# Performance work log

Hardware: AMD Instinct MI355X
Metric: run time of the kernel (lower is better)

## Reference

```python
import jax, jax.numpy as jnp
import numpy as np

BS, T, G, C = 64, 128, 36, 256
H = 256          # gaze LSTM hidden
P = 256          # spatial projected size
PT = 256         # temporal projected size
Q = 16           # queue size
NC = 10          # num classes
NEG = -1e9


def setup_inputs() -> dict:
    key = jax.random.key(0)
    ks = jax.random.split(key, 40)
    s = 0.02
    D = C + H
    inp = {
        'cnn_feat_seq': jax.random.normal(ks[0], (BS, T, G, C), jnp.float32),
        'gaze_seq': jax.random.normal(ks[1], (BS, T, 3), jnp.float32),
        # init-hidden / init-cell MLPs (Linear(3,H), Tanh, Linear(H,H), Tanh)
        'init_h_w1': jax.random.normal(ks[2], (H, 3)) * s, 'init_h_b1': jnp.zeros((H,)),
        'init_h_w2': jax.random.normal(ks[3], (H, H)) * s, 'init_h_b2': jnp.zeros((H,)),
        'init_c_w1': jax.random.normal(ks[4], (H, 3)) * s, 'init_c_b1': jnp.zeros((H,)),
        'init_c_w2': jax.random.normal(ks[5], (H, H)) * s, 'init_c_b2': jnp.zeros((H,)),
        # LSTM (input 3, hidden H), torch gate order i,f,g,o
        'lstm_wih': jax.random.normal(ks[6], (4 * H, 3)) * s, 'lstm_whh': jax.random.normal(ks[7], (4 * H, H)) * s,
        'lstm_bih': jnp.zeros((4 * H,)), 'lstm_bhh': jnp.zeros((4 * H,)),
        # spatial attention
        'sa_wl': jax.random.normal(ks[8], (P, H)) * s, 'sa_bl': jnp.zeros((P,)),
        'sa_wc': jax.random.normal(ks[9], (P, C)) * s, 'sa_bc': jnp.zeros((P,)),
        'sa_wz': jax.random.normal(ks[10], (P,)) * s,
        # temporal attention
        'ta_wl': jax.random.normal(ks[11], (PT, H)) * s, 'ta_bl': jnp.zeros((PT,)),
        'ta_wv': jax.random.normal(ks[12], (PT, C)) * s, 'ta_bv': jnp.zeros((PT,)),
        'ta_wz': jax.random.normal(ks[13], (PT,)) * s,
        # MLP classifier: Linear(D,D) -> Linear(D,D) -> Linear(D,NC), no nonlinearity
        'mlp_w1': jax.random.normal(ks[14], (D, D)) * s, 'mlp_b1': jnp.zeros((D,)),
        'mlp_w2': jax.random.normal(ks[15], (D, D)) * s, 'mlp_b2': jnp.zeros((D,)),
        'mlp_w3': jax.random.normal(ks[16], (NC, D)) * s, 'mlp_b3': jnp.zeros((NC,)),
    }
    return inp


def _forward(cnn_feat_seq, gaze_seq,
             init_h_w1, init_h_b1, init_h_w2, init_h_b2,
             init_c_w1, init_c_b1, init_c_w2, init_c_b2,
             lstm_wih, lstm_whh, lstm_bih, lstm_bhh,
             sa_wl, sa_bl, sa_wc, sa_bc, sa_wz,
             ta_wl, ta_bl, ta_wv, ta_bv, ta_wz,
             mlp_w1, mlp_b1, mlp_w2, mlp_b2, mlp_w3, mlp_b3):
    bs, num_frame = gaze_seq.shape[0], gaze_seq.shape[1]
    mean_gaze = jnp.mean(gaze_seq, axis=1)  # (bs, 3)
    # init MLP ends with Tanh, and forward applies F.tanh again
    h0 = jnp.tanh(jnp.tanh(jnp.tanh(mean_gaze @ init_h_w1.T + init_h_b1) @ init_h_w2.T + init_h_b2))
    c0 = jnp.tanh(jnp.tanh(jnp.tanh(mean_gaze @ init_c_w1.T + init_c_b1) @ init_c_w2.T + init_c_b2))
    buf_s0 = jnp.zeros((Q, bs, C), cnn_feat_seq.dtype)
    buf_h0 = jnp.zeros((Q, bs, H), cnn_feat_seq.dtype)
    qidx = jnp.arange(Q)

    def step(carry, xs):
        h, c, buf_s, buf_h, i = carry
        feat, gaze = xs  # (bs,G,C), (bs,3)
        # --- spatial additive attention over grids ---
        Hp = h @ sa_wl.T + sa_bl                                  # (bs,P)
        Vp = jnp.einsum('bgc,pc->bgp', feat, sa_wc) + sa_bc       # (bs,G,P)
        zs = jnp.tanh(Hp[:, None, :] + Vp) @ sa_wz                # (bs,G)
        sw = jax.nn.softmax(zs, axis=1)
        spat = jnp.einsum('bgc,bg->bc', feat, sw)                 # (bs,C)
        # --- rolling queues (newest last) ---
        buf_s = jnp.concatenate([buf_s[1:], spat[None]], axis=0)
        buf_h = jnp.concatenate([buf_h[1:], h[None]], axis=0)
        count = jnp.minimum(i + 1, Q)
        mask = qidx >= (Q - count)                                # (Q,) valid slots
        # --- temporal additive attention over queue ---
        Hq = jnp.einsum('qbh,ph->qbp', buf_h, ta_wl) + ta_bl
        Vq = jnp.einsum('qbc,pc->qbp', buf_s, ta_wv) + ta_bv
        zt = jnp.tanh(Hq + Vq) @ ta_wz                            # (Q,bs)
        zt = jnp.where(mask[:, None], zt, NEG)
        tw = jax.nn.softmax(zt, axis=0)
        temp = jnp.einsum('qbc,qb->bc', buf_s, tw)                # (bs,C)
        # --- one LSTM step on gaze ---
        gates = gaze @ lstm_wih.T + lstm_bih + h @ lstm_whh.T + lstm_bhh
        gi, gf, gg, go = jnp.split(gates, 4, axis=-1)
        c = jax.nn.sigmoid(gf) * c + jax.nn.sigmoid(gi) * jnp.tanh(gg)
        h = jax.nn.sigmoid(go) * jnp.tanh(c)
        # --- classifier on concat(temporal_feat, lstm_hidden) ---
        fc = jnp.concatenate([temp, h], axis=1)                   # (bs, C+H)
        pred = ((fc @ mlp_w1.T + mlp_b1) @ mlp_w2.T + mlp_b2) @ mlp_w3.T + mlp_b3
        return (h, c, buf_s, buf_h, i + 1), pred

    feats_t = jnp.swapaxes(cnn_feat_seq, 0, 1)  # (T,bs,G,C)
    gaze_t = jnp.swapaxes(gaze_seq, 0, 1)       # (T,bs,3)
    _, preds = jax.lax.scan(step, (h0, c0, buf_s0, buf_h0, jnp.int32(0)), (feats_t, gaze_t))
    # torch cats (1,bs,NC) pieces along dim=1 -> (1, T*bs, NC)
    return preds.reshape(1, num_frame * bs, NC)


def reference(cnn_feat_seq, gaze_seq,
              init_h_w1, init_h_b1, init_h_w2, init_h_b2,
              init_c_w1, init_c_b1, init_c_w2, init_c_b2,
              lstm_wih, lstm_whh, lstm_bih, lstm_bhh,
              sa_wl, sa_bl, sa_wc, sa_bc, sa_wz,
              ta_wl, ta_bl, ta_wv, ta_bv, ta_wz,
              mlp_w1, mlp_b1, mlp_w2, mlp_b2, mlp_w3, mlp_b3):
    return _forward(cnn_feat_seq, gaze_seq,
                    init_h_w1, init_h_b1, init_h_w2, init_h_b2,
                    init_c_w1, init_c_b1, init_c_w2, init_c_b2,
                    lstm_wih, lstm_whh, lstm_bih, lstm_bhh,
                    sa_wl, sa_bl, sa_wc, sa_bc, sa_wz,
                    ta_wl, ta_bl, ta_wv, ta_bv, ta_wz,
                    mlp_w1, mlp_b1, mlp_w2, mlp_b2, mlp_w3, mlp_b3)
```

## Files before the change

### kernel.cpp

```cpp
#include <hip/hip_runtime.h>
#include <cstdint>
#include <cstddef>

#define BSZ 64
#define TT  128
#define GG  36
#define CC  256
#define HH  256
#define QQ  16
#define NCLS 10
#define NROW 8192
#define SP_ROWS 16

using short8  = __attribute__((ext_vector_type(8))) short;
using f32x4   = __attribute__((ext_vector_type(4))) float;
using half2_t = __attribute__((ext_vector_type(2))) _Float16;
typedef unsigned int u32;
typedef unsigned short u16;

#define OFF_WI    0u
#define OFF_WF    131072u
#define OFF_WG    262144u
#define OFF_WO    393216u
#define OFF_SAWL  524288u
#define OFF_TAWL  655360u
#define OFF_TAWV  786432u
#define OFF_SAWC  917504u
#define OFF_W32   1048576u
#define OFF_WC    1069056u
#define OFF_BC    1089536u
#define OFF_H0F16 1089792u
#define OFF_C0    1122560u
#define OFF_HSEQ  1188096u
#define OFF_HSEQB 9642240u
#define OFF_HPSA  13869312u
#define OFF_HQ    22257920u
#define OFF_SPAT  30646528u
#define OFF_SPATB 39035136u
#define OFF_ZSC   43229440u
#define WS_NEEDED 43262208u
#define OFF_FEATB 43262208u
#define WS_NEED_BIG 194257152u

__device__ __forceinline__ float rcp_fast(float x){
#if __has_builtin(__builtin_amdgcn_rcpf)
  return __builtin_amdgcn_rcpf(x);
#else
  return 1.f/x;
#endif
}
__device__ __forceinline__ float fast_sig(float x){ return rcp_fast(1.f+__expf(-x)); }
__device__ __forceinline__ float fast_tanh(float x){ float e=__expf(2.f*x); return 1.f-2.f*rcp_fast(e+1.f); }
__device__ __forceinline__ u16 f2bf(float f){
  u32 u = __builtin_bit_cast(u32, f);
  u += 0x7fffu + ((u>>16)&1u);
  return (u16)(u>>16);
}
__device__ __forceinline__ float bf2f(u16 b){
  u32 u = ((u32)b)<<16; return __builtin_bit_cast(float, u);
}
__device__ __forceinline__ u32 cvtpk_bf16(float a, float b){
  u32 p;
  asm("v_cvt_pk_bf16_f32 %0, %1, %2" : "=v"(p) : "v"(a), "v"(b));
  return p;
}
__device__ __forceinline__ u32 packf16(float a, float b){
  half2_t h; h.x = (_Float16)a; h.y = (_Float16)b;
  return __builtin_bit_cast(u32, h);
}
__device__ __forceinline__ float dot2(u32 w, u32 h, float acc){
#if __has_builtin(__builtin_amdgcn_fdot2)
  return __builtin_amdgcn_fdot2(__builtin_bit_cast(half2_t, w),
                                __builtin_bit_cast(half2_t, h), acc, false);
#else
  half2_t a = __builtin_bit_cast(half2_t, w), b = __builtin_bit_cast(half2_t, h);
  return acc + (float)a.x*(float)b.x + (float)a.y*(float)b.y;
#endif
}
__device__ __forceinline__ f32x4 mfma16(short8 a, short8 b, f32x4 c){
  return __builtin_amdgcn_mfma_f32_16x16x32_bf16(a, b, c, 0, 0, 0);
}

__global__ void __launch_bounds__(256) k_prep1(const float* __restrict__ whh,
    const float* __restrict__ sawl, const float* __restrict__ tawl,
    const float* __restrict__ tawv, const float* __restrict__ sawc,
    const float* __restrict__ w3, const float* __restrict__ w2, char* ws){
  int blk = blockIdx.x, tid = threadIdx.x;
  if (blk < 512){
    u32* wq = (u32*)ws;
    for (int rr = 0; rr < 2; ++rr){
      int row = blk*2 + rr;
      float v  = whh[row*256 + tid];
      float vn = __shfl_down(v, 1);
      if ((tid & 1) == 0){
        int typ = row >> 8;
        int j   = row & 255;
        wq[typ*32768 + (tid>>1)*256 + j] = packf16(v, vn);
      }
    }
  } else if (blk < 544){
    int rel = blk - 512;
    int mat = rel >> 3;
    const float* src; u16* dst;
    if (mat==0){ src=sawl; dst=(u16*)(ws+OFF_SAWL); }
    else if (mat==1){ src=tawl; dst=(u16*)(ws+OFF_TAWL); }
    else if (mat==2){ src=tawv; dst=(u16*)(ws+OFF_TAWV); }
    else { src=sawc; dst=(u16*)(ws+OFF_SAWC); }
    int base = (rel & 7)*8192 + tid;
    if (mat < 3){
      for (int i = 0; i < 32; ++i){ int e = base + i*256; dst[e] = f2bf(src[e]); }
    } else {
      for (int i = 0; i < 32; ++i){
        int e = base + i*256;
        int col = e >> 8, kk = e & 255;
        dst[col*256 + (kk ^ ((col&7)<<3))] = f2bf(src[e]);
      }
    }
  } else {
    int idx = (blk-544)*256 + tid;
    int o = idx >> 9, k2 = idx & 511;
    float acc = 0.f;
    for (int m = 0; m < 512; ++m) acc = fmaf(w3[o*512+m], w2[m*512+k2], acc);
    ((float*)(ws+OFF_W32))[idx] = acc;
  }
}

__global__ void __launch_bounds__(256) k_prep2(const float* __restrict__ w1,
    const float* __restrict__ b1, const float* __restrict__ w3,
    const float* __restrict__ b2, const float* __restrict__ b3,
    const float* __restrict__ gaze,
    const float* __restrict__ ihw1, const float* __restrict__ ihb1,
    const float* __restrict__ ihw2, const float* __restrict__ ihb2,
    const float* __restrict__ icw1, const float* __restrict__ icb1,
    const float* __restrict__ icw2, const float* __restrict__ icb2,
    char* ws){
  int blk = blockIdx.x, tid = threadIdx.x;
  const float* W32 = (const float*)(ws+OFF_W32);
  if (blk < 20){
    int idx = blk*256 + tid; int o = idx>>9, k = idx&511;
    float acc = 0.f;
    for (int m = 0; m < 512; ++m) acc = fmaf(W32[o*512+m], w1[m*512+k], acc);
    ((float*)(ws+OFF_WC))[idx] = acc;
  } else if (blk == 20){
    if (tid < 10){
      float acc = b3[tid];
      for (int m = 0; m < 512; ++m) acc = fmaf(W32[tid*512+m], b1[m], acc);
      for (int m = 0; m < 512; ++m) acc = fmaf(w3[tid*512+m], b2[m], acc);
      ((float*)(ws+OFF_BC))[tid] = acc;
    }
  } else {
    int b = blk - 21;
    __shared__ float red0[128], red1[128], red2[128];
    __shared__ float mg[3];
    __shared__ float x1[256];
    if (tid < 128){
      const float* gp = gaze + b*384 + tid*3;
      red0[tid] = gp[0]; red1[tid] = gp[1]; red2[tid] = gp[2];
    }
    __syncthreads();
    for (int s = 64; s >= 1; s >>= 1){
      if (tid < s){ red0[tid]+=red0[tid+s]; red1[tid]+=red1[tid+s]; red2[tid]+=red2[tid+s]; }
      __syncthreads();
    }
    if (tid == 0){ mg[0]=red0[0]*(1.f/128.f); mg[1]=red1[0]*(1.f/128.f); mg[2]=red2[0]*(1.f/128.f); }
    __syncthreads();
    for (int which = 0; which < 2; ++which){
      const float* aw1 = which? icw1 : ihw1; const float* ab1 = which? icb1 : ihb1;
      const float* aw2 = which? icw2 : ihw2; const float* ab2 = which? icb2 : ihb2;
      float v = fast_tanh(fmaf(aw1[tid*3+2],mg[2], fmaf(aw1[tid*3+1],mg[1], fmaf(aw1[tid*3],mg[0], ab1[tid]))));
      x1[tid] = v;
      __syncthreads();
      float acc = ab2[tid];
      for (int k = 0; k < 256; ++k) acc = fmaf(aw2[tid*256+k], x1[k], acc);
      float h0 = fast_tanh(fast_tanh(acc));
      if (which == 0){
        float* hseq = (float*)(ws+OFF_HSEQ);
        hseq[(size_t)(0*64 + b)*256 + tid] = h0;
        float hn = __shfl_down(h0, 1);
        if ((tid&1)==0){
          ((u32*)(ws+OFF_HSEQB))[((size_t)(0*64+b)*256 + tid)>>1] = ((u32)f2bf(hn)<<16) | f2bf(h0);
          ((u32*)(ws+OFF_H0F16))[b*128 + (tid>>1)] = packf16(h0, hn);
        }
      } else {
        ((float*)(ws+OFF_C0))[b*256 + tid] = h0;
      }
      __syncthreads();
    }
  }
}

__global__ void __launch_bounds__(512, 2) k_lstm_vp(const float* __restrict__ gaze,
    const float* __restrict__ wih, const float* __restrict__ bih,
    const float* __restrict__ bhh, const float* __restrict__ feat, char* ws){
  __shared__ u32 lds_w[16*2048];
  __shared__ __align__(16) u32 hbuf[2][128];
  __shared__ float p_lds[256];
  __shared__ float g_lds[384];
  int tid = threadIdx.x;

  if (blockIdx.x >= 64){
    int cb = blockIdx.x - 64;
    u32* fbg = (u32*)(ws + OFF_FEATB);
    for (int r = cb; r < NROW; r += 192){
      int t = r >> 6, b = r & 63;
      const float4* fb = (const float4*)(feat + ((size_t)(b*128 + t))*9216);
      u32* dst = fbg + (size_t)r*4608;
#pragma unroll
      for (int ii = 0; ii < 4; ++ii){
        int e = tid + ii*512;
        float4 v = fb[e];
        int g = e >> 6, c4 = e & 63;
        uint2 pp;
        pp.x = cvtpk_bf16(v.x, v.y);
        pp.y = cvtpk_bf16(v.z, v.w);
        *reinterpret_cast<uint2*>(dst + g*128 + ((c4*2) ^ ((g&7)<<2))) = pp;
      }
      if (tid < 256){
        int e = 2048 + tid;
        float4 v = fb[e];
        int g = e >> 6, c4 = e & 63;
        uint2 pp;
        pp.x = cvtpk_bf16(v.x, v.y);
        pp.y = cvtpk_bf16(v.z, v.w);
        *reinterpret_cast<uint2*>(dst + g*128 + ((c4*2) ^ ((g&7)<<2))) = pp;
      }
    }
    return;
  }

  int b = blockIdx.x;
  int half = tid >> 8;
  int j = tid & 255;

  const u32* wq = (const u32*)ws;
  const u32* wA = wq + (half ? 1 : 0) * 32768;
  const u32* wB = wq + (half ? 3 : 2) * 32768;
  u32 w0[128], w1r[64];
#pragma unroll
  for (int c = 0; c < 128; ++c) w0[c] = wA[c*256 + j];
#pragma unroll
  for (int c = 0; c < 64; ++c)  w1r[c] = wB[c*256 + j];
#pragma unroll
  for (int cq = 0; cq < 16; ++cq)
#pragma unroll
    for (int q = 0; q < 4; ++q)
      lds_w[cq*2048 + tid*4 + q] = wB[(64 + cq*4 + q)*256 + j];

  if (tid < 384) g_lds[tid] = gaze[b*384 + tid];
  if (tid < 128) hbuf[0][tid] = ((const u32*)(ws+OFF_H0F16))[b*128 + tid];
  float creg = half ? ((const float*)(ws+OFF_C0))[b*256 + j] : 0.f;

  int rA = half ? 256 + j : j;
  int rB = half ? 768 + j : 512 + j;
  float baseA = bih[rA] + bhh[rA];
  float baseB = bih[rB] + bhh[rB];
  float uA0 = wih[rA*3], uA1 = wih[rA*3+1], uA2 = wih[rA*3+2];
  float uB0 = wih[rB*3], uB1 = wih[rB*3+1], uB2 = wih[rB*3+2];

  float* hseq = (float*)(ws+OFF_HSEQ);
  u32* hseqb = (u32*)(ws+OFF_HSEQB);
  float hv_prev = 0.f; u32 hpk_prev = 0;
  __syncthreads();

  for (int t = 0; t < 128; ++t){
    int cur = t & 1, nxt = cur ^ 1;
    if (half == 1 && t > 0){
      hseq[((size_t)t*64 + b)*256 + j] = hv_prev;
      if ((j & 1) == 0)
        hseqb[(((size_t)t*64 + b)*256 + j)>>1] = hpk_prev;
    }
    float g0 = g_lds[t*3], g1 = g_lds[t*3+1], g2 = g_lds[t*3+2];
    float aA0 = fmaf(uA2,g2, fmaf(uA1,g1, fmaf(uA0,g0, baseA))), aA1 = 0.f;
    float aB0 = fmaf(uB2,g2, fmaf(uB1,g1, fmaf(uB0,g0, baseB))), aB1 = 0.f;
#pragma unroll
    for (int c4 = 0; c4 < 32; ++c4){
      uint4 h4 = *reinterpret_cast<const uint4*>(&hbuf[cur][c4*4]);
      u32 wb0, wb1, wb2, wb3;
      if (c4 < 16){
        wb0 = w1r[c4*4]; wb1 = w1r[c4*4+1]; wb2 = w1r[c4*4+2]; wb3 = w1r[c4*4+3];
      } else {
        uint4 wv = *reinterpret_cast<const uint4*>(&lds_w[(c4-16)*2048 + tid*4]);
        wb0 = wv.x; wb1 = wv.y; wb2 = wv.z; wb3 = wv.w;
      }
      aA0 = dot2(w0[c4*4+0], h4.x, aA0); aB0 = dot2(wb0, h4.x, aB0);
      aA1 = dot2(w0[c4*4+1], h4.y, aA1); aB1 = dot2(wb1, h4.y, aB1);
      aA0 = dot2(w0[c4*4+2], h4.z, aA0); aB0 = dot2(wb2, h4.z, aB0);
      aA1 = dot2(w0[c4*4+3], h4.w, aA1); aB1 = dot2(wb3, h4.w, aB1);
    }
    float aA = aA0 + aA1, aB = aB0 + aB1;
    if (half == 0){
      p_lds[j] = fast_sig(aA) * fast_tanh(aB);
    }
    __syncthreads();
    if (half == 1){
      float p = p_lds[j];
      creg = fmaf(fast_sig(aA), creg, p);
      float hv = fast_sig(aB) * fast_tanh(creg);
      float hn = __shfl_down(hv, 1);
      if ((j & 1) == 0) hbuf[nxt][j>>1] = packf16(hv, hn);
      hv_prev = hv;
      hpk_prev = ((u32)f2bf(hn)<<16) | f2bf(hv);
    }
    __syncthreads();
  }
  if (half == 1){
    hseq[((size_t)128*64 + b)*256 + j] = hv_prev;
    if ((j & 1) == 0)
      hseqb[(((size_t)128*64 + b)*256 + j)>>1] = hpk_prev;
  }
}

__global__ void __launch_bounds__(512, 2) k_lstm(const float* __restrict__ gaze,
    const float* __restrict__ wih, const float* __restrict__ bih,
    const float* __restrict__ bhh, char* ws){
  int b = blockIdx.x, tid = threadIdx.x;
  int half = tid >> 8;
  int j = tid & 255;
  __shared__ u32 lds_w[16*2048];
  __shared__ __align__(16) u32 hbuf[2][128];
  __shared__ float p_lds[256];
  __shared__ float g_lds[384];

  const u32* wq = (const u32*)ws;
  const u32* wA = wq + (half ? 1 : 0) * 32768;
  const u32* wB = wq + (half ? 3 : 2) * 32768;
  u32 w0[128], w1r[64];
#pragma unroll
  for (int c = 0; c < 128; ++c) w0[c] = wA[c*256 + j];
#pragma unroll
  for (int c = 0; c < 64; ++c)  w1r[c] = wB[c*256 + j];
#pragma unroll
  for (int cq = 0; cq < 16; ++cq)
#pragma unroll
    for (int q = 0; q < 4; ++q)
      lds_w[cq*2048 + tid*4 + q] = wB[(64 + cq*4 + q)*256 + j];

  if (tid < 384) g_lds[tid] = gaze[b*384 + tid];
  if (tid < 128) hbuf[0][tid] = ((const u32*)(ws+OFF_H0F16))[b*128 + tid];
  float creg = half ? ((const float*)(ws+OFF_C0))[b*256 + j] : 0.f;

  int rA = half ? 256 + j : j;
  int rB = half ? 768 + j : 512 + j;
  float baseA = bih[rA] + bhh[rA];
  float baseB = bih[rB] + bhh[rB];
  float uA0 = wih[rA*3], uA1 = wih[rA*3+1], uA2 = wih[rA*3+2];
  float uB0 = wih[rB*3], uB1 = wih[rB*3+1], uB2 = wih[rB*3+2];

  float* hseq = (float*)(ws+OFF_HSEQ);
  u32* hseqb = (u32*)(ws+OFF_HSEQB);
  float hv_prev = 0.f; u32 hpk_prev = 0;
  __syncthreads();

  for (int t = 0; t < 128; ++t){
    int cur = t & 1, nxt = cur ^ 1;
    if (half == 1 && t > 0){
      hseq[((size_t)t*64 + b)*256 + j] = hv_prev;
      if ((j & 1) == 0)
        hseqb[(((size_t)t*64 + b)*256 + j)>>1] = hpk_prev;
    }
    float g0 = g_lds[t*3], g1 = g_lds[t*3+1], g2 = g_lds[t*3+2];
    float aA0 = fmaf(uA2,g2, fmaf(uA1,g1, fmaf(uA0,g0, baseA))), aA1 = 0.f;
    float aB0 = fmaf(uB2,g2, fmaf(uB1,g1, fmaf(uB0,g0, baseB))), aB1 = 0.f;
#pragma unroll
    for (int c4 = 0; c4 < 32; ++c4){
      uint4 h4 = *reinterpret_cast<const uint4*>(&hbuf[cur][c4*4]);
      u32 wb0, wb1, wb2, wb3;
      if (c4 < 16){
        wb0 = w1r[c4*4]; wb1 = w1r[c4*4+1]; wb2 = w1r[c4*4+2]; wb3 = w1r[c4*4+3];
      } else {
        uint4 wv = *reinterpret_cast<const uint4*>(&lds_w[(c4-16)*2048 + tid*4]);
        wb0 = wv.x; wb1 = wv.y; wb2 = wv.z; wb3 = wv.w;
      }
      aA0 = dot2(w0[c4*4+0], h4.x, aA0); aB0 = dot2(wb0, h4.x, aB0);
      aA1 = dot2(w0[c4*4+1], h4.y, aA1); aB1 = dot2(wb1, h4.y, aB1);
      aA0 = dot2(w0[c4*4+2], h4.z, aA0); aB0 = dot2(wb2, h4.z, aB0);
      aA1 = dot2(w0[c4*4+3], h4.w, aA1); aB1 = dot2(wb3, h4.w, aB1);
    }
    float aA = aA0 + aA1, aB = aB0 + aB1;
    if (half == 0){
      p_lds[j] = fast_sig(aA) * fast_tanh(aB);
    }
    __syncthreads();
    if (half == 1){
      float p = p_lds[j];
      creg = fmaf(fast_sig(aA), creg, p);
      float hv = fast_sig(aB) * fast_tanh(creg);
      float hn = __shfl_down(hv, 1);
      if ((j & 1) == 0) hbuf[nxt][j>>1] = packf16(hv, hn);
      hv_prev = hv;
      hpk_prev = ((u32)f2bf(hn)<<16) | f2bf(hv);
    }
    __syncthreads();
  }
  if (half == 1){
    hseq[((size_t)128*64 + b)*256 + j] = hv_prev;
    if ((j & 1) == 0)
      hseqb[(((size_t)128*64 + b)*256 + j)>>1] = hpk_prev;
  }
}

__global__ void __launch_bounds__(256) k_proj1(const float* __restrict__ sabl,
    const float* __restrict__ sabc, const float* __restrict__ tabl,
    const float* __restrict__ tabv, char* ws){
  int bx = blockIdx.x, which = blockIdx.y;
  const u16* A = (const u16*)(ws+OFF_HSEQB);
  const u16* B = (const u16*)(ws + (which? OFF_TAWL : OFF_SAWL));
  float* Out   = (float*)(ws + (which? OFF_HQ : OFF_HPSA));
  const float* bp1 = which? tabl : sabl;
  const float* bp2 = which? tabv : sabc;
  int tid = threadIdx.x, w = tid>>6, l = tid&63;
  int lr = l&15, lk = l>>4;
  int rb = bx*64;
  short8 afr[4][8];
#pragma unroll
  for (int m = 0; m < 4; ++m)
#pragma unroll
    for (int k = 0; k < 8; ++k)
      afr[m][k] = *(const short8*)(const void*)(A + (size_t)(rb + m*16 + lr)*256 + k*32 + lk*8);
#pragma unroll
  for (int n = 0; n < 4; ++n){
    int cb = w*64 + n*16;
    int col = cb + lr;
    float bias = bp1[col] + bp2[col];
    f32x4 a0 = {0.f,0.f,0.f,0.f}, a1 = a0, a2 = a0, a3 = a0;
#pragma unroll
    for (int k = 0; k < 8; ++k){
      short8 bf = *(const short8*)(const void*)(B + (size_t)col*256 + k*32 + lk*8);
      a0 = mfma16(afr[0][k], bf, a0);
      a1 = mfma16(afr[1][k], bf, a1);
      a2 = mfma16(afr[2][k], bf, a2);
      a3 = mfma16(afr[3][k], bf, a3);
    }
#pragma unroll
    for (int q = 0; q < 4; ++q){
      Out[(size_t)(rb + 0*16 + lk*4 + q)*256 + col] = a0[q] + bias;
      Out[(size_t)(rb + 1*16 + lk*4 + q)*256 + col] = a1[q] + bias;
      Out[(size_t)(rb + 2*16 + lk*4 + q)*256 + col] = a2[q] + bias;
      Out[(size_t)(rb + 3*16 + lk*4 + q)*256 + col] = a3[q] + bias;
    }
  }
}

__global__ void __launch_bounds__(512, 2) k_spatial_fin(const float* __restrict__ sawz,
    char* ws){
  __shared__ __align__(16) u16 featb[48*256];
  __shared__ __align__(16) float hp[256];
  __shared__ float wzs[256];
  __shared__ float zsbuf[8][48];
  __shared__ float swl[36];
  __shared__ float psum[2][256];
  int bx = blockIdx.x, tid = threadIdx.x, w = tid>>6, l = tid&63;
  int lr = l&15, lk = l>>4;
  int colbase = w*32;
  const float* hpsa = (const float*)(ws+OFF_HPSA);
  const u16* Bw = (const u16*)(ws+OFF_SAWC);
  const uint2* fbg = (const uint2*)(ws + OFF_FEATB);

  short8 breg[2][8];
#pragma unroll
  for (int n = 0; n < 2; ++n){
    int col = colbase + n*16 + lr;
#pragma unroll
    for (int k = 0; k < 8; ++k)
      breg[n][k] = *(const short8*)(const void*)(Bw + (size_t)col*256 + ((k*32 + lk*8) ^ ((col&7)<<3)));
  }
  if (tid < 256) wzs[tid] = sawz[tid];

  uint2 pf2[5]; float4 ph;
  {
    int r0 = bx*SP_ROWS;
    const uint2* src = fbg + (size_t)r0*2304;
#pragma unroll
    for (int ii = 0; ii < 4; ++ii) pf2[ii] = src[tid + ii*512];
    if (tid < 256) pf2[4] = src[2048 + tid];
    if (tid < 64) ph = ((const float4*)(hpsa + (size_t)r0*256))[tid];
  }
  __syncthreads();

  for (int i = 0; i < SP_ROWS; ++i){
    int r = bx*SP_ROWS + i;
    {
      uint2* lds2 = (uint2*)featb;
#pragma unroll
      for (int ii = 0; ii < 4; ++ii) lds2[tid + ii*512] = pf2[ii];
      if (tid < 256) lds2[2048 + tid] = pf2[4];
      if (tid < 64) *reinterpret_cast<float4*>(hp + tid*4) = ph;
    }
    __syncthreads();
    if (i + 1 < SP_ROWS){
      int rn = r + 1;
      const uint2* src = fbg + (size_t)rn*2304;
#pragma unroll
      for (int ii = 0; ii < 4; ++ii) pf2[ii] = src[tid + ii*512];
      if (tid < 256) pf2[4] = src[2048 + tid];
      if (tid < 64) ph = ((const float4*)(hpsa + (size_t)rn*256))[tid];
    }
    float zacc[3][4] = {{0.f}};
#pragma unroll
    for (int m = 0; m < 3; ++m){
      short8 afr[8];
#pragma unroll
      for (int k = 0; k < 8; ++k){
        int g = m*16 + lr;
        afr[k] = *(const short8*)(const void*)(featb + g*256 + ((k*32 + lk*8) ^ ((g&7)<<3)));
      }
#pragma unroll
      for (int n = 0; n < 2; ++n){
        f32x4 a = {0.f,0.f,0.f,0.f};
#pragma unroll
        for (int k = 0; k < 8; ++k) a = mfma16(afr[k], breg[n][k], a);
        int col = colbase + n*16 + lr;
        float hpl = hp[col], wzv = wzs[col];
#pragma unroll
        for (int q = 0; q < 4; ++q)
          zacc[m][q] += fast_tanh(a[q] + hpl)*wzv;
      }
    }
#pragma unroll
    for (int m = 0; m < 3; ++m)
#pragma unroll
      for (int q = 0; q < 4; ++q){
        float v = zacc[m][q];
        v += __shfl_xor(v, 1); v += __shfl_xor(v, 2);
        v += __shfl_xor(v, 4); v += __shfl_xor(v, 8);
        if (lr == 0) zsbuf[w][m*16 + lk*4 + q] = v;
      }
    __syncthreads();
    if (w == 0){
      float z = -1e30f;
      if (l < 36)
        z = zsbuf[0][l]+zsbuf[1][l]+zsbuf[2][l]+zsbuf[3][l]
          + zsbuf[4][l]+zsbuf[5][l]+zsbuf[6][l]+zsbuf[7][l];
      float mx = z;
      for (int d = 1; d < 64; d <<= 1) mx = fmaxf(mx, __shfl_xor(mx, d));
      float e = (l < 36)? __expf(z - mx) : 0.f;
      float s = e;
      for (int d = 1; d < 64; d <<= 1) s += __shfl_xor(s, d);
      if (l < 36) swl[l] = e * rcp_fast(s);
    }
    __syncthreads();
    {
      int hsel = tid >> 8, col = tid & 255;
      float part = 0.f;
#pragma unroll
      for (int gg = 0; gg < 18; ++gg){
        int g = hsel*18 + gg;
        part = fmaf(swl[g], bf2f(featb[g*256 + (col ^ ((g&7)<<3))]), part);
      }
      psum[hsel][col] = part;
    }
    __syncthreads();
    if (tid < 256){
      float acc = psum[0][tid] + psum[1][tid];
      ((float*)(ws+OFF_SPAT))[(size_t)r*256 + tid] = acc;
      float an = __shfl_down(acc, 1);
      if ((tid & 1) == 0)
        ((u32*)(ws+OFF_SPATB))[((size_t)r*256 + tid)>>1] = cvtpk_bf16(acc, an);
    }
  }
}

__global__ void __launch_bounds__(512, 2) k_spatial(const float* __restrict__ feat,
    const float* __restrict__ sawz, char* ws){
  __shared__ __align__(16) u16 featb[48*256];
  __shared__ __align__(16) float hp[256];
  __shared__ float wzs[256];
  __shared__ float zsbuf[8][48];
  __shared__ float swl[36];
  __shared__ float psum[2][256];
  int bx = blockIdx.x, tid = threadIdx.x, w = tid>>6, l = tid&63;
  int lr = l&15, lk = l>>4;
  int colbase = w*32;
  const float* hpsa = (const float*)(ws+OFF_HPSA);
  const u16* Bw = (const u16*)(ws+OFF_SAWC);

  short8 breg[2][8];
#pragma unroll
  for (int n = 0; n < 2; ++n){
    int col = colbase + n*16 + lr;
#pragma unroll
    for (int k = 0; k < 8; ++k)
      breg[n][k] = *(const short8*)(const void*)(Bw + (size_t)col*256 + ((k*32 + lk*8) ^ ((col&7)<<3)));
  }
  if (tid < 256) wzs[tid] = sawz[tid];

  float4 pf[5]; float4 ph;
  {
    int r0 = bx*SP_ROWS;
    int t = r0>>6, b = r0&63;
    const float4* fb = (const float4*)(feat + ((size_t)(b*128 + t))*9216);
#pragma unroll
    for (int ii = 0; ii < 4; ++ii) pf[ii] = fb[tid + ii*512];
    if (tid < 256) pf[4] = fb[2048 + tid];
    if (tid < 64) ph = ((const float4*)(hpsa + (size_t)r0*256))[tid];
  }
  __syncthreads();

  for (int i = 0; i < SP_ROWS; ++i){
    int r = bx*SP_ROWS + i;
#pragma unroll
    for (int ii = 0; ii < 4; ++ii){
      int e = tid + ii*512;
      int g = e >> 6, c4 = e & 63;
      uint2 pp;
      pp.x = cvtpk_bf16(pf[ii].x, pf[ii].y);
      pp.y = cvtpk_bf16(pf[ii].z, pf[ii].w);
      *reinterpret_cast<uint2*>((u32*)featb + g*128 + ((c4*2) ^ ((g&7)<<2))) = pp;
    }
    if (tid < 256){
      int e = 2048 + tid;
      int g = e >> 6, c4 = e & 63;
      uint2 pp;
      pp.x = cvtpk_bf16(pf[4].x, pf[4].y);
      pp.y = cvtpk_bf16(pf[4].z, pf[4].w);
      *reinterpret_cast<uint2*>((u32*)featb + g*128 + ((c4*2) ^ ((g&7)<<2))) = pp;
    }
    if (tid < 64) *reinterpret_cast<float4*>(hp + tid*4) = ph;
    __syncthreads();
    if (i + 1 < SP_ROWS){
      int rn = r + 1;
      int t = rn>>6, b = rn&63;
      const float4* fb = (const float4*)(feat + ((size_t)(b*128 + t))*9216);
#pragma unroll
      for (int ii = 0; ii < 4; ++ii) pf[ii] = fb[tid + ii*512];
      if (tid < 256) pf[4] = fb[2048 + tid];
      if (tid < 64) ph = ((const float4*)(hpsa + (size_t)rn*256))[tid];
    }
    float zacc[3][4] = {{0.f}};
#pragma unroll
    for (int m = 0; m < 3; ++m){
      short8 afr[8];
#pragma unroll
      for (int k = 0; k < 8; ++k){
        int g = m*16 + lr;
        afr[k] = *(const short8*)(const void*)(featb + g*256 + ((k*32 + lk*8) ^ ((g&7)<<3)));
      }
#pragma unroll
      for (int n = 0; n < 2; ++n){
        f32x4 a = {0.f,0.f,0.f,0.f};
#pragma unroll
        for (int k = 0; k < 8; ++k) a = mfma16(afr[k], breg[n][k], a);
        int col = colbase + n*16 + lr;
        float hpl = hp[col], wzv = wzs[col];
#pragma unroll
        for (int q = 0; q < 4; ++q)
          zacc[m][q] += fast_tanh(a[q] + hpl)*wzv;
      }
    }
#pragma unroll
    for (int m = 0; m < 3; ++m)
#pragma unroll
      for (int q = 0; q < 4; ++q){
        float v = zacc[m][q];
        v += __shfl_xor(v, 1); v += __shfl_xor(v, 2);
        v += __shfl_xor(v, 4); v += __shfl_xor(v, 8);
        if (lr == 0) zsbuf[w][m*16 + lk*4 + q] = v;
      }
    __syncthreads();
    if (w == 0){
      float z = -1e30f;
      if (l < 36)
        z = zsbuf[0][l]+zsbuf[1][l]+zsbuf[2][l]+zsbuf[3][l]
          + zsbuf[4][l]+zsbuf[5][l]+zsbuf[6][l]+zsbuf[7][l];
      float mx = z;
      for (int d = 1; d < 64; d <<= 1) mx = fmaxf(mx, __shfl_xor(mx, d));
      float e = (l < 36)? __expf(z - mx) : 0.f;
      float s = e;
      for (int d = 1; d < 64; d <<= 1) s += __shfl_xor(s, d);
      if (l < 36) swl[l] = e * rcp_fast(s);
    }
    __syncthreads();
    {
      int hsel = tid >> 8, col = tid & 255;
      float part = 0.f;
#pragma unroll
      for (int gg = 0; gg < 18; ++gg){
        int g = hsel*18 + gg;
        part = fmaf(swl[g], bf2f(featb[g*256 + (col ^ ((g&7)<<3))]), part);
      }
      psum[hsel][col] = part;
    }
    __syncthreads();
    if (tid < 256){
      float acc = psum[0][tid] + psum[1][tid];
      ((float*)(ws+OFF_SPAT))[(size_t)r*256 + tid] = acc;
      float an = __shfl_down(acc, 1);
      if ((tid & 1) == 0)
        ((u32*)(ws+OFF_SPATB))[((size_t)r*256 + tid)>>1] = cvtpk_bf16(acc, an);
    }
  }
}

__global__ void __launch_bounds__(256) k_proj2(const float* __restrict__ tawz, char* ws){
  int bx = blockIdx.x;
  int tid = threadIdx.x, w = tid>>6, l = tid&63;
  int lr = l&15, lk = l>>4;
  int rb = bx*64;
  const u16* A = (const u16*)(ws+OFF_SPATB);
  const u16* B = (const u16*)(ws+OFF_TAWV);
  const float* Hq = (const float*)(ws+OFF_HQ);
  __shared__ float zbuf[4][64];
  short8 afr[4][8];
#pragma unroll
  for (int m = 0; m < 4; ++m)
#pragma unroll
    for (int k = 0; k < 8; ++k)
      afr[m][k] = *(const short8*)(const void*)(A + (size_t)(rb + m*16 + lr)*256 + k*32 + lk*8);
  float racc[4][4] = {{0.f}};
#pragma unroll
  for (int n = 0; n < 4; ++n){
    int col = w*64 + n*16 + lr;
    float tzl = tawz[col];
    f32x4 a0 = {0.f,0.f,0.f,0.f}, a1 = a0, a2 = a0, a3 = a0;
#pragma unroll
    for (int k = 0; k < 8; ++k){
      short8 bf = *(const short8*)(const void*)(B + (size_t)col*256 + k*32 + lk*8);
      a0 = mfma16(afr[0][k], bf, a0);
      a1 = mfma16(afr[1][k], bf, a1);
      a2 = mfma16(afr[2][k], bf, a2);
      a3 = mfma16(afr[3][k], bf, a3);
    }
#pragma unroll
    for (int q = 0; q < 4; ++q){
      racc[0][q] += fast_tanh(a0[q] + Hq[(size_t)(rb + 0*16 + lk*4 + q)*256 + col]) * tzl;
      racc[1][q] += fast_tanh(a1[q] + Hq[(size_t)(rb + 1*16 + lk*4 + q)*256 + col]) * tzl;
      racc[2][q] += fast_tanh(a2[q] + Hq[(size_t)(rb + 2*16 + lk*4 + q)*256 + col]) * tzl;
      racc[3][q] += fast_tanh(a3[q] + Hq[(size_t)(rb + 3*16 + lk*4 + q)*256 + col]) * tzl;
    }
  }
#pragma unroll
  for (int m = 0; m < 4; ++m)
#pragma unroll
    for (int q = 0; q < 4; ++q){
      float v = racc[m][q];
      v += __shfl_xor(v, 1); v += __shfl_xor(v, 2);
      v += __shfl_xor(v, 4); v += __shfl_xor(v, 8);
      if (lr == 0) zbuf[w][m*16 + lk*4 + q] = v;
    }
  __syncthreads();
  if (tid < 64)
    ((float*)(ws+OFF_ZSC))[rb + tid] = zbuf[0][tid]+zbuf[1][tid]+zbuf[2][tid]+zbuf[3][tid];
}

__global__ void __launch_bounds__(256) k_final(float* __restrict__ out, char* ws){
  int bx = blockIdx.x;
  int b = bx & 63, tb = bx >> 6;
  int t0 = tb*8;
  int tid = threadIdx.x;
  int wv = tid>>6, l = tid&63;
  __shared__ float spw[23][256];
  __shared__ float zw[23];
  __shared__ float WcL[5120];
  __shared__ float bcL[10];
  __shared__ float w16[16];
  __shared__ float wpart[4][10];
  const float* spat = (const float*)(ws+OFF_SPAT);
  const float* zsc  = (const float*)(ws+OFF_ZSC);
  const float* hseq = (const float*)(ws+OFF_HSEQ);
  const float* Wc   = (const float*)(ws+OFF_WC);
#pragma unroll
  for (int i = 0; i < 20; ++i) WcL[tid + i*256] = Wc[tid + i*256];
  if (tid < 10) bcL[tid] = ((const float*)(ws+OFF_BC))[tid];
  for (int i = 0; i < 23; ++i){
    int tau = t0 - 15 + i;
    spw[i][tid] = (tau >= 0)? spat[(size_t)(tau*64 + b)*256 + tid] : 0.f;
  }
  if (tid < 23){
    int tau = t0 - 15 + tid;
    zw[tid] = (tau >= 0)? zsc[tau*64 + b] : -1e9f;
  }
  __syncthreads();
  for (int dt = 0; dt < 8; ++dt){
    int t = t0 + dt;
    if (wv == 0 && l < 16){
      float z = zw[dt + l];
      float mx = z;
      mx = fmaxf(mx, __shfl_xor(mx,1)); mx = fmaxf(mx, __shfl_xor(mx,2));
      mx = fmaxf(mx, __shfl_xor(mx,4)); mx = fmaxf(mx, __shfl_xor(mx,8));
      float e = __expf(z - mx);
      float s = e;
      s += __shfl_xor(s,1); s += __shfl_xor(s,2); s += __shfl_xor(s,4); s += __shfl_xor(s,8);
      w16[l] = e / s;
    }
    __syncthreads();
    float temp = 0.f;
#pragma unroll
    for (int qi = 0; qi < 16; ++qi) temp = fmaf(w16[qi], spw[dt+qi][tid], temp);
    float hc = hseq[(size_t)((t+1)*64 + b)*256 + tid];
    float po[10];
#pragma unroll
    for (int o = 0; o < 10; ++o){
      float v = fmaf(temp, WcL[o*512 + tid], hc*WcL[o*512 + 256 + tid]);
      v += __shfl_xor(v,1);  v += __shfl_xor(v,2);  v += __shfl_xor(v,4);
      v += __shfl_xor(v,8);  v += __shfl_xor(v,16); v += __shfl_xor(v,32);
      po[o] = v;
    }
    if (l == 0){
#pragma unroll
      for (int o = 0; o < 10; ++o) wpart[wv][o] = po[o];
    }
    __syncthreads();
    if (tid < 10)
      out[(size_t)(t*64 + b)*10 + tid] = wpart[0][tid]+wpart[1][tid]+wpart[2][tid]+wpart[3][tid] + bcL[tid];
    __syncthreads();
  }
}

extern "C" void kernel_launch(void* const* d_in, const int* in_sizes, int n_in,
                              void* d_out, int out_size, void* d_ws, size_t ws_size,
                              hipStream_t stream){
  const float* feat = (const float*)d_in[0];
  const float* gaze = (const float*)d_in[1];
  const float* ihw1 = (const float*)d_in[2];  const float* ihb1 = (const float*)d_in[3];
  const float* ihw2 = (const float*)d_in[4];  const float* ihb2 = (const float*)d_in[5];
  const float* icw1 = (const float*)d_in[6];  const float* icb1 = (const float*)d_in[7];
  const float* icw2 = (const float*)d_in[8];  const float* icb2 = (const float*)d_in[9];
  const float* wih  = (const float*)d_in[10]; const float* whh  = (const float*)d_in[11];
  const float* bih  = (const float*)d_in[12]; const float* bhh  = (const float*)d_in[13];
  const float* sawl = (const float*)d_in[14]; const float* sabl = (const float*)d_in[15];
  const float* sawc = (const float*)d_in[16]; const float* sabc = (const float*)d_in[17];
  const float* sawz = (const float*)d_in[18];
  const float* tawl = (const float*)d_in[19]; const float* tabl = (const float*)d_in[20];
  const float* tawv = (const float*)d_in[21]; const float* tabv = (const float*)d_in[22];
  const float* tawz = (const float*)d_in[23];
  const float* w1 = (const float*)d_in[24]; const float* b1 = (const float*)d_in[25];
  const float* w2 = (const float*)d_in[26]; const float* b2 = (const float*)d_in[27];
  const float* w3 = (const float*)d_in[28]; const float* b3 = (const float*)d_in[29];
  char* ws = (char*)d_ws;
  float* out = (float*)d_out;
  if (ws_size < (size_t)WS_NEEDED) return;
  bool big = ws_size >= (size_t)WS_NEED_BIG;

  k_prep1<<<dim3(564), dim3(256), 0, stream>>>(whh, sawl, tawl, tawv, sawc, w3, w2, ws);
  k_prep2<<<dim3(85), dim3(256), 0, stream>>>(w1, b1, w3, b2, b3, gaze,
      ihw1, ihb1, ihw2, ihb2, icw1, icb1, icw2, icb2, ws);
  if (big){
    k_lstm_vp<<<dim3(256), dim3(512), 0, stream>>>(gaze, wih, bih, bhh, feat, ws);
    k_proj1<<<dim3(128, 2), dim3(256), 0, stream>>>(sabl, sabc, tabl, tabv, ws);
    k_spatial_fin<<<dim3(512), dim3(512), 0, stream>>>(sawz, ws);
  } else {
    k_lstm<<<dim3(64), dim3(512), 0, stream>>>(gaze, wih, bih, bhh, ws);
    k_proj1<<<dim3(128, 2), dim3(256), 0, stream>>>(sabl, sabc, tabl, tabv, ws);
    k_spatial<<<dim3(512), dim3(512), 0, stream>>>(feat, sawz, ws);
  }
  k_proj2<<<dim3(128), dim3(256), 0, stream>>>(tawz, ws);
  k_final<<<dim3(1024), dim3(256), 0, stream>>>(out, ws);
}
```

Measured before the change: 503.0 us.

## Split spatial attention into score kernel and separate softmax weighted-sum kernel

```diff
diff --git a/kernel.cpp b/kernel.cpp
--- a/kernel.cpp
+++ b/kernel.cpp
@@ -40,7 +40,8 @@
 #define OFF_ZSC   43229440u
 #define WS_NEEDED 43262208u
 #define OFF_FEATB 43262208u
-#define WS_NEED_BIG 194257152u
+#define OFF_ZS    194257152u
+#define WS_NEED_BIG 195436800u
 
 __device__ __forceinline__ float rcp_fast(float x){
 #if __has_builtin(__builtin_amdgcn_rcpf)
@@ -200,29 +201,27 @@
 
   if (blockIdx.x >= 64){
     int cb = blockIdx.x - 64;
-    u32* fbg = (u32*)(ws + OFF_FEATB);
+    uint2* fbg = (uint2*)(ws + OFF_FEATB);
     for (int r = cb; r < NROW; r += 192){
       int t = r >> 6, b = r & 63;
       const float4* fb = (const float4*)(feat + ((size_t)(b*128 + t))*9216);
-      u32* dst = fbg + (size_t)r*4608;
+      uint2* dst = fbg + (size_t)r*2304;
 #pragma unroll
       for (int ii = 0; ii < 4; ++ii){
         int e = tid + ii*512;
         float4 v = fb[e];
-        int g = e >> 6, c4 = e & 63;
         uint2 pp;
         pp.x = cvtpk_bf16(v.x, v.y);
         pp.y = cvtpk_bf16(v.z, v.w);
-        *reinterpret_cast<uint2*>(dst + g*128 + ((c4*2) ^ ((g&7)<<2))) = pp;
+        dst[e] = pp;
       }
       if (tid < 256){
         int e = 2048 + tid;
         float4 v = fb[e];
-        int g = e >> 6, c4 = e & 63;
         uint2 pp;
         pp.x = cvtpk_bf16(v.x, v.y);
         pp.y = cvtpk_bf16(v.z, v.w);
-        *reinterpret_cast<uint2*>(dst + g*128 + ((c4*2) ^ ((g&7)<<2))) = pp;
+        dst[e] = pp;
       }
     }
     return;
@@ -441,20 +440,19 @@
   }
 }
 
-__global__ void __launch_bounds__(512, 2) k_spatial_fin(const float* __restrict__ sawz,
+__global__ void __launch_bounds__(512, 2) k_zspat(const float* __restrict__ sawz,
     char* ws){
-  __shared__ __align__(16) u16 featb[48*256];
-  __shared__ __align__(16) float hp[256];
+  __shared__ __align__(16) u16 featb[2][48*256];
+  __shared__ __align__(16) float hp[2][256];
   __shared__ float wzs[256];
-  __shared__ float zsbuf[8][48];
-  __shared__ float swl[36];
-  __shared__ float psum[2][256];
+  __shared__ float zsbuf[2][8][48];
   int bx = blockIdx.x, tid = threadIdx.x, w = tid>>6, l = tid&63;
   int lr = l&15, lk = l>>4;
   int colbase = w*32;
   const float* hpsa = (const float*)(ws+OFF_HPSA);
   const u16* Bw = (const u16*)(ws+OFF_SAWC);
-  const uint2* fbg = (const uint2*)(ws + OFF_FEATB);
+  const uint4* fbg4 = (const uint4*)(ws + OFF_FEATB);
+  float* zs = (float*)(ws+OFF_ZS);
 
   short8 breg[2][8];
 #pragma unroll
@@ -466,35 +464,32 @@
   }
   if (tid < 256) wzs[tid] = sawz[tid];
 
-  uint2 pf2[5]; float4 ph;
+  uint4 pf[3]; float4 ph;
   {
     int r0 = bx*SP_ROWS;
-    const uint2* src = fbg + (size_t)r0*2304;
-#pragma unroll
-    for (int ii = 0; ii < 4; ++ii) pf2[ii] = src[tid + ii*512];
-    if (tid < 256) pf2[4] = src[2048 + tid];
+    const uint4* src = fbg4 + (size_t)r0*1152;
+    pf[0] = src[tid]; pf[1] = src[tid+512];
+    if (tid < 128) pf[2] = src[1024+tid];
     if (tid < 64) ph = ((const float4*)(hpsa + (size_t)r0*256))[tid];
   }
-  __syncthreads();
 
   for (int i = 0; i < SP_ROWS; ++i){
-    int r = bx*SP_ROWS + i;
+    int cur = i & 1;
     {
-      uint2* lds2 = (uint2*)featb;
-#pragma unroll
-      for (int ii = 0; ii < 4; ++ii) lds2[tid + ii*512] = pf2[ii];
-      if (tid < 256) lds2[2048 + tid] = pf2[4];
-      if (tid < 64) *reinterpret_cast<float4*>(hp + tid*4) = ph;
-    }
-    __syncthreads();
+      uint4* db = (uint4*)featb[cur];
+      int j0 = tid;       { int g=j0>>5, wi=j0&31; db[g*32 + (wi ^ (g&7))] = pf[0]; }
+      int j1 = tid + 512; { int g=j1>>5, wi=j1&31; db[g*32 + (wi ^ (g&7))] = pf[1]; }
+      if (tid < 128){ int j2 = 1024 + tid; int g=j2>>5, wi=j2&31; db[g*32 + (wi ^ (g&7))] = pf[2]; }
+      if (tid < 64) *reinterpret_cast<float4*>(&hp[cur][tid*4]) = ph;
+    }
     if (i + 1 < SP_ROWS){
-      int rn = r + 1;
-      const uint2* src = fbg + (size_t)rn*2304;
-#pragma unroll
-      for (int ii = 0; ii < 4; ++ii) pf2[ii] = src[tid + ii*512];
-      if (tid < 256) pf2[4] = src[2048 + tid];
+      int rn = bx*SP_ROWS + i + 1;
+      const uint4* src = fbg4 + (size_t)rn*1152;
+      pf[0] = src[tid]; pf[1] = src[tid+512];
+      if (tid < 128) pf[2] = src[1024+tid];
       if (tid < 64) ph = ((const float4*)(hpsa + (size_t)rn*256))[tid];
     }
+    __syncthreads();
     float zacc[3][4] = {{0.f}};
 #pragma unroll
     for (int m = 0; m < 3; ++m){
@@ -502,7 +497,7 @@
 #pragma unroll
       for (int k = 0; k < 8; ++k){
         int g = m*16 + lr;
-        afr[k] = *(const short8*)(const void*)(featb + g*256 + ((k*32 + lk*8) ^ ((g&7)<<3)));
+        afr[k] = *(const short8*)(const void*)(featb[cur] + g*256 + ((k*32 + lk*8) ^ ((g&7)<<3)));
       }
 #pragma unroll
       for (int n = 0; n < 2; ++n){
@@ -510,7 +505,7 @@
 #pragma unroll
         for (int k = 0; k < 8; ++k) a = mfma16(afr[k], breg[n][k], a);
         int col = colbase + n*16 + lr;
-        float hpl = hp[col], wzv = wzs[col];
+        float hpl = hp[cur][col], wzv = wzs[col];
 #pragma unroll
         for (int q = 0; q < 4; ++q)
           zacc[m][q] += fast_tanh(a[q] + hpl)*wzv;
@@ -523,41 +518,47 @@
         float v = zacc[m][q];
         v += __shfl_xor(v, 1); v += __shfl_xor(v, 2);
         v += __shfl_xor(v, 4); v += __shfl_xor(v, 8);
-        if (lr == 0) zsbuf[w][m*16 + lk*4 + q] = v;
-      }
-    __syncthreads();
-    if (w == 0){
-      float z = -1e30f;
-      if (l < 36)
-        z = zsbuf[0][l]+zsbuf[1][l]+zsbuf[2][l]+zsbuf[3][l]
-          + zsbuf[4][l]+zsbuf[5][l]+zsbuf[6][l]+zsbuf[7][l];
-      float mx = z;
-      for (int d = 1; d < 64; d <<= 1) mx = fmaxf(mx, __shfl_xor(mx, d));
-      float e = (l < 36)? __expf(z - mx) : 0.f;
-      float s = e;
-      for (int d = 1; d < 64; d <<= 1) s += __shfl_xor(s, d);
-      if (l < 36) swl[l] = e * rcp_fast(s);
-    }
-    __syncthreads();
-    {
-      int hsel = tid >> 8, col = tid & 255;
-      float part = 0.f;
-#pragma unroll
-      for (int gg = 0; gg < 18; ++gg){
-        int g = hsel*18 + gg;
-        part = fmaf(swl[g], bf2f(featb[g*256 + (col ^ ((g&7)<<3))]), part);
-      }
-      psum[hsel][col] = part;
-    }
-    __syncthreads();
-    if (tid < 256){
-      float acc = psum[0][tid] + psum[1][tid];
-      ((float*)(ws+OFF_SPAT))[(size_t)r*256 + tid] = acc;
-      float an = __shfl_down(acc, 1);
-      if ((tid & 1) == 0)
-        ((u32*)(ws+OFF_SPATB))[((size_t)r*256 + tid)>>1] = cvtpk_bf16(acc, an);
-    }
-  }
+        if (lr == 0) zsbuf[cur][w][m*16 + lk*4 + q] = v;
+      }
+    if (w == 0 && i > 0 && l < 36){
+      int prev = cur ^ 1;
+      float s = zsbuf[prev][0][l] + zsbuf[prev][1][l] + zsbuf[prev][2][l] + zsbuf[prev][3][l]
+              + zsbuf[prev][4][l] + zsbuf[prev][5][l] + zsbuf[prev][6][l] + zsbuf[prev][7][l];
+      zs[(size_t)(bx*SP_ROWS + i - 1)*36 + l] = s;
+    }
+  }
+  __syncthreads();
+  if (w == 0 && l < 36){
+    int prev = (SP_ROWS - 1) & 1;
+    float s = zsbuf[prev][0][l] + zsbuf[prev][1][l] + zsbuf[prev][2][l] + zsbuf[prev][3][l]
+            + zsbuf[prev][4][l] + zsbuf[prev][5][l] + zsbuf[prev][6][l] + zsbuf[prev][7][l];
+    zs[(size_t)(bx*SP_ROWS + SP_ROWS - 1)*36 + l] = s;
+  }
+}
+
+__global__ void __launch_bounds__(256) k_wsum(char* ws){
+  __shared__ float swl[36];
+  int r = blockIdx.x, tid = threadIdx.x, w = tid>>6, l = tid&63;
+  const float* zs = (const float*)(ws+OFF_ZS);
+  const u16* fb = (const u16*)(ws+OFF_FEATB) + (size_t)r*9216;
+  if (w == 0){
+    float z = (l < 36)? zs[(size_t)r*36 + l] : -1e30f;
+    float mx = z;
+    for (int d = 1; d < 64; d <<= 1) mx = fmaxf(mx, __shfl_xor(mx, d));
+    float e = (l < 36)? __expf(z - mx) : 0.f;
+    float s = e;
+    for (int d = 1; d < 64; d <<= 1) s += __shfl_xor(s, d);
+    if (l < 36) swl[l] = e * rcp_fast(s);
+  }
+  __syncthreads();
+  float acc = 0.f;
+#pragma unroll
+  for (int g = 0; g < 36; ++g)
+    acc = fmaf(swl[g], bf2f(fb[g*256 + tid]), acc);
+  ((float*)(ws+OFF_SPAT))[(size_t)r*256 + tid] = acc;
+  float an = __shfl_down(acc, 1);
+  if ((tid & 1) == 0)
+    ((u32*)(ws+OFF_SPATB))[((size_t)r*256 + tid)>>1] = cvtpk_bf16(acc, an);
 }
 
 __global__ void __launch_bounds__(512, 2) k_spatial(const float* __restrict__ feat,
@@ -837,7 +838,8 @@
   if (big){
     k_lstm_vp<<<dim3(256), dim3(512), 0, stream>>>(gaze, wih, bih, bhh, feat, ws);
     k_proj1<<<dim3(128, 2), dim3(256), 0, stream>>>(sabl, sabc, tabl, tabv, ws);
-    k_spatial_fin<<<dim3(512), dim3(512), 0, stream>>>(sawz, ws);
+    k_zspat<<<dim3(512), dim3(512), 0, stream>>>(sawz, ws);
+    k_wsum<<<dim3(8192), dim3(256), 0, stream>>>(ws);
   } else {
     k_lstm<<<dim3(64), dim3(512), 0, stream>>>(gaze, wih, bih, bhh, ws);
     k_proj1<<<dim3(128, 2), dim3(256), 0, stream>>>(sabl, sabc, tabl, tabv, ws);
```

Result: slower. 541.6 us (+7.7%).

## Widen spatial attention kernel to 1024 threads with double-buffered LDS tiles

Applied to the files above, without the earlier changes.

```diff
diff --git a/kernel.cpp b/kernel.cpp
--- a/kernel.cpp
+++ b/kernel.cpp
@@ -200,29 +200,27 @@
 
   if (blockIdx.x >= 64){
     int cb = blockIdx.x - 64;
-    u32* fbg = (u32*)(ws + OFF_FEATB);
+    uint2* fbg = (uint2*)(ws + OFF_FEATB);
     for (int r = cb; r < NROW; r += 192){
       int t = r >> 6, b = r & 63;
       const float4* fb = (const float4*)(feat + ((size_t)(b*128 + t))*9216);
-      u32* dst = fbg + (size_t)r*4608;
+      uint2* dst = fbg + (size_t)r*2304;
 #pragma unroll
       for (int ii = 0; ii < 4; ++ii){
         int e = tid + ii*512;
         float4 v = fb[e];
-        int g = e >> 6, c4 = e & 63;
         uint2 pp;
         pp.x = cvtpk_bf16(v.x, v.y);
         pp.y = cvtpk_bf16(v.z, v.w);
-        *reinterpret_cast<uint2*>(dst + g*128 + ((c4*2) ^ ((g&7)<<2))) = pp;
+        dst[e] = pp;
       }
       if (tid < 256){
         int e = 2048 + tid;
         float4 v = fb[e];
-        int g = e >> 6, c4 = e & 63;
         uint2 pp;
         pp.x = cvtpk_bf16(v.x, v.y);
         pp.y = cvtpk_bf16(v.z, v.w);
-        *reinterpret_cast<uint2*>(dst + g*128 + ((c4*2) ^ ((g&7)<<2))) = pp;
+        dst[e] = pp;
       }
     }
     return;
@@ -441,80 +439,78 @@
   }
 }
 
-__global__ void __launch_bounds__(512, 2) k_spatial_fin(const float* __restrict__ sawz,
+__global__ void __launch_bounds__(1024, 4) k_spatial_big(const float* __restrict__ sawz,
     char* ws){
-  __shared__ __align__(16) u16 featb[48*256];
-  __shared__ __align__(16) float hp[256];
+  __shared__ __align__(16) u16 featb[2][48*256];
+  __shared__ float hp[2][256];
   __shared__ float wzs[256];
-  __shared__ float zsbuf[8][48];
+  __shared__ float zsbuf[16][48];
   __shared__ float swl[36];
-  __shared__ float psum[2][256];
+  __shared__ float psum[4][256];
   int bx = blockIdx.x, tid = threadIdx.x, w = tid>>6, l = tid&63;
   int lr = l&15, lk = l>>4;
-  int colbase = w*32;
+  int colbase = w*16;
   const float* hpsa = (const float*)(ws+OFF_HPSA);
   const u16* Bw = (const u16*)(ws+OFF_SAWC);
-  const uint2* fbg = (const uint2*)(ws + OFF_FEATB);
-
-  short8 breg[2][8];
-#pragma unroll
-  for (int n = 0; n < 2; ++n){
-    int col = colbase + n*16 + lr;
+  const uint4* fbg4 = (const uint4*)(ws + OFF_FEATB);
+
+  short8 breg[8];
+  {
+    int col = colbase + lr;
 #pragma unroll
     for (int k = 0; k < 8; ++k)
-      breg[n][k] = *(const short8*)(const void*)(Bw + (size_t)col*256 + ((k*32 + lk*8) ^ ((col&7)<<3)));
+      breg[k] = *(const short8*)(const void*)(Bw + (size_t)col*256 + ((k*32 + lk*8) ^ ((col&7)<<3)));
   }
   if (tid < 256) wzs[tid] = sawz[tid];
 
-  uint2 pf2[5]; float4 ph;
+  uint4 pf0, pf1; float hpn = 0.f;
   {
     int r0 = bx*SP_ROWS;
-    const uint2* src = fbg + (size_t)r0*2304;
-#pragma unroll
-    for (int ii = 0; ii < 4; ++ii) pf2[ii] = src[tid + ii*512];
-    if (tid < 256) pf2[4] = src[2048 + tid];
-    if (tid < 64) ph = ((const float4*)(hpsa + (size_t)r0*256))[tid];
-  }
-  __syncthreads();
+    const uint4* src = fbg4 + (size_t)r0*1152;
+    pf0 = src[tid];
+    if (tid < 128) pf1 = src[1024 + tid];
+    if (tid < 256) hpn = hpsa[(size_t)r0*256 + tid];
+  }
 
   for (int i = 0; i < SP_ROWS; ++i){
+    int cur = i & 1;
     int r = bx*SP_ROWS + i;
     {
-      uint2* lds2 = (uint2*)featb;
-#pragma unroll
-      for (int ii = 0; ii < 4; ++ii) lds2[tid + ii*512] = pf2[ii];
-      if (tid < 256) lds2[2048 + tid] = pf2[4];
-      if (tid < 64) *reinterpret_cast<float4*>(hp + tid*4) = ph;
-    }
-    __syncthreads();
+      uint4* db = (uint4*)featb[cur];
+      { int g = tid>>5, wi = tid&31; db[g*32 + (wi ^ (g&7))] = pf0; }
+      if (tid < 128){ int j1 = 1024 + tid; int g = j1>>5, wi = j1&31; db[g*32 + (wi ^ (g&7))] = pf1; }
+      if (tid < 256) hp[cur][tid] = hpn;
+    }
     if (i + 1 < SP_ROWS){
       int rn = r + 1;
-      const uint2* src = fbg + (size_t)rn*2304;
-#pragma unroll
-      for (int ii = 0; ii < 4; ++ii) pf2[ii] = src[tid + ii*512];
-      if (tid < 256) pf2[4] = src[2048 + tid];
-      if (tid < 64) ph = ((const float4*)(hpsa + (size_t)rn*256))[tid];
-    }
+      const uint4* src = fbg4 + (size_t)rn*1152;
+      pf0 = src[tid];
+      if (tid < 128) pf1 = src[1024 + tid];
+      if (tid < 256) hpn = hpsa[(size_t)rn*256 + tid];
+    }
+    __syncthreads();
     float zacc[3][4] = {{0.f}};
+    float hpl = hp[cur][colbase + lr];
+    float wzv = wzs[colbase + lr];
 #pragma unroll
     for (int m = 0; m < 3; ++m){
-      short8 afr[8];
-#pragma unroll
-      for (int k = 0; k < 8; ++k){
-        int g = m*16 + lr;
-        afr[k] = *(const short8*)(const void*)(featb + g*256 + ((k*32 + lk*8) ^ ((g&7)<<3)));
-      }
-#pragma unroll
-      for (int n = 0; n < 2; ++n){
-        f32x4 a = {0.f,0.f,0.f,0.f};
-#pragma unroll
-        for (int k = 0; k < 8; ++k) a = mfma16(afr[k], breg[n][k], a);
-        int col = colbase + n*16 + lr;
-        float hpl = hp[col], wzv = wzs[col];
-#pragma unroll
-        for (int q = 0; q < 4; ++q)
-          zacc[m][q] += fast_tanh(a[q] + hpl)*wzv;
-      }
+      f32x4 a = {0.f,0.f,0.f,0.f};
+#pragma unroll
+      for (int kh = 0; kh < 2; ++kh){
+        short8 afr4[4];
+#pragma unroll
+        for (int k4 = 0; k4 < 4; ++k4){
+          int g = m*16 + lr;
+          int koff = (kh*4 + k4)*32 + lk*8;
+          afr4[k4] = *(const short8*)(const void*)(featb[cur] + g*256 + (koff ^ ((g&7)<<3)));
+        }
+#pragma unroll
+        for (int k4 = 0; k4 < 4; ++k4)
+          a = mfma16(afr4[k4], breg[kh*4 + k4], a);
+      }
+#pragma unroll
+      for (int q = 0; q < 4; ++q)
+        zacc[m][q] += fast_tanh(a[q] + hpl)*wzv;
     }
 #pragma unroll
     for (int m = 0; m < 3; ++m)
@@ -528,9 +524,11 @@
     __syncthreads();
     if (w == 0){
       float z = -1e30f;
-      if (l < 36)
-        z = zsbuf[0][l]+zsbuf[1][l]+zsbuf[2][l]+zsbuf[3][l]
-          + zsbuf[4][l]+zsbuf[5][l]+zsbuf[6][l]+zsbuf[7][l];
+      if (l < 36){
+        z = 0.f;
+#pragma unroll
+        for (int ww = 0; ww < 16; ++ww) z += zsbuf[ww][l];
+      }
       float mx = z;
       for (int d = 1; d < 64; d <<= 1) mx = fmaxf(mx, __shfl_xor(mx, d));
       float e = (l < 36)? __expf(z - mx) : 0.f;
@@ -543,20 +541,21 @@
       int hsel = tid >> 8, col = tid & 255;
       float part = 0.f;
 #pragma unroll
-      for (int gg = 0; gg < 18; ++gg){
-        int g = hsel*18 + gg;
-        part = fmaf(swl[g], bf2f(featb[g*256 + (col ^ ((g&7)<<3))]), part);
+      for (int gg = 0; gg < 9; ++gg){
+        int g = hsel*9 + gg;
+        part = fmaf(swl[g], bf2f(featb[cur][g*256 + (col ^ ((g&7)<<3))]), part);
       }
       psum[hsel][col] = part;
     }
     __syncthreads();
     if (tid < 256){
-      float acc = psum[0][tid] + psum[1][tid];
+      float acc = psum[0][tid] + psum[1][tid] + psum[2][tid] + psum[3][tid];
       ((float*)(ws+OFF_SPAT))[(size_t)r*256 + tid] = acc;
       float an = __shfl_down(acc, 1);
       if ((tid & 1) == 0)
         ((u32*)(ws+OFF_SPATB))[((size_t)r*256 + tid)>>1] = cvtpk_bf16(acc, an);
     }
+    __syncthreads();
   }
 }
 
@@ -837,7 +836,7 @@
   if (big){
     k_lstm_vp<<<dim3(256), dim3(512), 0, stream>>>(gaze, wih, bih, bhh, feat, ws);
     k_proj1<<<dim3(128, 2), dim3(256), 0, stream>>>(sabl, sabc, tabl, tabv, ws);
-    k_spatial_fin<<<dim3(512), dim3(512), 0, stream>>>(sawz, ws);
+    k_spatial_big<<<dim3(512), dim3(1024), 0, stream>>>(sawz, ws);
   } else {
     k_lstm<<<dim3(64), dim3(512), 0, stream>>>(gaze, wih, bih, bhh, ws);
     k_proj1<<<dim3(128, 2), dim3(256), 0, stream>>>(sabl, sabc, tabl, tabv, ws);
```

Result: slower. 534.8 us (+6.3%).
